# Optimization experiments

Measured on AMD Instinct MI355X. Metric: run time of the kernel, lower is better.

## Reference

```python
import jax, jax.numpy as jnp
import numpy as np

# Fixed hyperparameters from init_kwargs
KH, KW = 3, 3
GRID_SIZE = 5
SPLINE_ORDER = 3
GRID_RANGE = (-1.0, 1.0)


def _make_grid():
    # grid buffer: arange(-k, grid_size + k + 1) * h + grid_range[0], shape (G + 2k + 1,) = (12,)
    h = (GRID_RANGE[1] - GRID_RANGE[0]) / GRID_SIZE
    return (jnp.arange(-SPLINE_ORDER, GRID_SIZE + SPLINE_ORDER + 1, dtype=jnp.float32) * h
            + GRID_RANGE[0])


def _unfold(x):
    # torch.nn.Unfold with kernel (3,3), stride 1, pad 0, dilation 1.
    # Returns (N, C*KH*KW) with channel-major ordering (c, i, j), matching torch.
    B, C, H, W = x.shape
    Ho, Wo = H - KH + 1, W - KW + 1
    cols = [x[:, :, i:i + Ho, j:j + Wo] for i in range(KH) for j in range(KW)]
    p = jnp.stack(cols, axis=2)                    # (B, C, KH*KW, Ho, Wo)
    p = p.reshape(B, C * KH * KW, Ho * Wo)         # (B, in_features, L)
    p = p.transpose(0, 2, 1).reshape(-1, C * KH * KW)  # (B*L, in_features)
    return p, Ho, Wo


def _b_splines(x, grid):
    # x: (N, in_features); grid: (G + 2k + 1,) uniform, shared across features.
    # Returns (N, in_features, G + k) B-spline basis via Cox-de Boor recursion.
    x = x[..., None]  # (N, in, 1)
    bases = ((x >= grid[:-1]) & (x < grid[1:])).astype(x.dtype)  # (N, in, G+2k)
    for k in range(1, SPLINE_ORDER + 1):
        left = (x - grid[: -(k + 1)]) / (grid[k:-1] - grid[: -(k + 1)])
        right = (grid[k + 1:] - x) / (grid[k + 1:] - grid[1:-k])
        bases = left * bases[..., :-1] + right * bases[..., 1:]
    return bases  # (N, in, G + k)


def setup_inputs() -> dict:
    key = jax.random.key(0)
    k1, k2, k3, k4 = jax.random.split(key, 4)
    in_features = 32 * KH * KW  # 288
    out_features = 64
    n_coef = GRID_SIZE + SPLINE_ORDER  # 8
    x = jax.random.normal(k1, (16, 32, 64, 64), dtype=jnp.float32)
    base_weight = jax.random.normal(k2, (out_features, in_features), dtype=jnp.float32) * (1.0 / np.sqrt(in_features))
    spline_weight = jax.random.normal(k3, (out_features, in_features, n_coef), dtype=jnp.float32) * 0.1
    spline_scaler = jax.random.normal(k4, (out_features, in_features), dtype=jnp.float32) * (1.0 / np.sqrt(in_features))
    return {"x": x, "base_weight": base_weight, "spline_weight": spline_weight,
            "spline_scaler": spline_scaler}


def reference(x, base_weight, spline_weight, spline_scaler):
    B = x.shape[0]
    out_features = base_weight.shape[0]
    grid = _make_grid()

    patches, Ho, Wo = _unfold(x)                              # (N, in_features)
    N, in_features = patches.shape

    # KANLinear forward
    base_out = jnp.matmul(jax.nn.relu(patches), base_weight.T)  # (N, out)
    bases = _b_splines(patches, grid)                           # (N, in, G+k)
    scaled_w = spline_weight * spline_scaler[..., None]         # (out, in, G+k)
    spline_out = jnp.matmul(bases.reshape(N, -1), scaled_w.reshape(out_features, -1).T)
    out = base_out + spline_out                                 # (N, out)

    out = out.reshape(B, Ho, Wo, out_features).transpose(0, 3, 1, 2)  # (B, C_out, Ho, Wo)
    return out
```

## Files before the change

kernel.cpp:

```cpp
#include <hip/hip_runtime.h>
#include <stdint.h>

typedef _Float16 half8  __attribute__((ext_vector_type(8)));
typedef float    f32x4  __attribute__((ext_vector_type(4)));
typedef float    f32x16 __attribute__((ext_vector_type(16)));
typedef uint32_t u32x4  __attribute__((ext_vector_type(4)));

#define FIN  288
#define NOUT 64
#define LPB  3844
#define NBF  20736
#define NBAS (16*64*16*64*2)
#define NXR  (16*64*2*64*2)
#define PADS 16

#define SCL  200
#define LDSL (31*SCL + 2*64 + 64 + 8)


__device__ inline half8 bspline8(float xv) {
  float u = fmaf(xv, 2.5f, 5.5f);
  float fi = floorf(u);
  int i = (int)fi;
  float t = u - fi, s = 1.0f - t;
  float t2 = t * t, t3 = t2 * t;
  float s2 = s * s, s3 = s2 * s;
  float w3 = t3 * 0.16666667f;
  float w0 = s3 * 0.16666667f;
  float w1 = fmaf(0.5f, t3, -t2) + 0.66666667f;
  float w2 = fmaf(0.5f, s3, -s2) + 0.66666667f;
  uint32_t u01 = __builtin_bit_cast(uint32_t, __builtin_amdgcn_cvt_pkrtz(w0, w1));
  uint32_t u23 = __builtin_bit_cast(uint32_t, __builtin_amdgcn_cvt_pkrtz(w2, w3));
  uint64_t V = (uint64_t)u01 | ((uint64_t)u23 << 32);
  uint32_t vl = (uint32_t)(V << 16);
  u32x4 fr;
#pragma unroll
  for (int q = 0; q < 4; ++q) {
    int d = i - 2 * q;
    uint32_t rr = (uint32_t)(V >> ((48 - 16 * d) & 63));
    fr[q] = ((uint32_t)d <= 3u) ? rr : ((d == 4) ? vl : 0u);
  }
  return __builtin_bit_cast(half8, fr);
}

__global__ __launch_bounds__(256) void prep_all(const float* __restrict__ x,
                                                const float* __restrict__ bw,
                                                const float* __restrict__ sw,
                                                const float* __restrict__ sc,
                                                half8* __restrict__ ws) {
  int bid = blockIdx.x;
  if (bid < 8192) {
    int t = bid * 256 + threadIdx.x;
    int half = t & 1;
    int w    = (t >> 1) & 63;
    int u    = (t >> 7) & 15;
    int bh   = t >> 11;
    float xv = x[(size_t)(bh >> 6) * 131072 + (u * 2 + half) * 4096 +
                 (bh & 63) * 64 + w];
    ws[NBF + t] = bspline8(xv);
  } else if (bid < 9216) {
    int t = (bid - 8192) * 256 + threadIdx.x;
    int half = t & 1;
    int w    = (t >> 1) & 63;
    int u    = (t >> 7) & 1;
    int bh   = t >> 8;
    const float* xp = x + (size_t)(bh >> 6) * 131072 + (u * 16 + half * 8) * 4096 +
                      (bh & 63) * 64 + w;
    half8 v;
#pragma unroll
    for (int j = 0; j < 8; ++j) v[j] = (_Float16)fmaxf(xp[j * 4096], 0.0f);
    ws[NBF + NBAS + t] = v;
  } else {
    int t = (bid - 9216) * 256 + threadIdx.x;
    half8 v;
    int dst;
    if (t < NOUT * FIN) {
      int o = t / FIN;
      int f = t - o * FIN;
      float scale = sc[t];
      const float* p = sw + t * 8;
#pragma unroll
      for (int j = 0; j < 8; ++j) v[j] = (_Float16)(p[j] * scale);
      int c  = f / 9;
      int r  = f - c * 9;
      int ii = r / 3;
      int jj = r - ii * 3;
      int pp = ii * 3 + jj;
      int u  = c >> 1, half = c & 1;
      int nf = o >> 5, col = o & 31;
      dst = pp * 2048 + u * 128 + nf * 64 + half * 32 + col;
    } else {
      int t2 = t - NOUT * FIN;
      int lane = t2 & 63;
      int nf   = (t2 >> 6) & 1;
      int u    = (t2 >> 7) & 1;
      int pos  = t2 >> 8;
      int half = lane >> 5, col = lane & 31;
      int o = nf * 32 + col;
#pragma unroll
      for (int j = 0; j < 8; ++j)
        v[j] = (_Float16)bw[o * FIN + 9 * (u * 16 + half * 8 + j) + pos];
      dst = NOUT * FIN + t2;
    }
    ws[dst] = v;
  }
}

#define MFMA32(A, B, C) __builtin_amdgcn_mfma_f32_32x32x16_f16((A), (B), (C), 0, 0, 0)

#define LOAD_AF(PP, AF)                                                     \
  {                                                                         \
    const half8* pAf_ = bbS + ((PP) / 3) * 2048 + ((PP) % 3) * 2;           \
    _Pragma("unroll")                                                       \
    for (int uu = 0; uu < 8; ++uu) {                                        \
      AF[uu * 2]     = pAf_[(ulo + uu) * 128];                              \
      AF[uu * 2 + 1] = pAf_[(ulo + uu) * 128 + 64];                         \
    }                                                                       \
  }

#define PAIR(PP, AFC, AFN)                                                  \
  {                                                                         \
    half8 stg[4];                                                           \
    if ((PP) < 8) {                                                         \
      const half8* src_ = bfrag + ((PP) + 1) * 2048;                        \
      _Pragma("unroll")                                                     \
      for (int i = 0; i < 4; ++i) stg[i] = src_[i * 512 + tid];             \
      LOAD_AF((PP) + 1, AFN)                                                \
    }                                                                       \
    _Pragma("unroll")                                                       \
    for (int uu = 0; uu < 8; ++uu) {                                        \
      int u_ = ulo + uu;                                                    \
      _Pragma("unroll")                                                     \
      for (int nf = 0; nf < 2; ++nf) {                                      \
        half8 bf_ = bcur[u_ * 128 + nf * 64 + lane];                        \
        acc[0][nf] = MFMA32(AFC[uu * 2], bf_, acc[0][nf]);                  \
        acc[1][nf] = MFMA32(AFC[uu * 2 + 1], bf_, acc[1][nf]);              \
      }                                                                     \
    }                                                                       \
    if ((PP) < 8) {                                                         \
      _Pragma("unroll")                                                     \
      for (int i = 0; i < 4; ++i) balt[i * 512 + tid] = stg[i];             \
    }                                                                       \
    __syncthreads();                                                        \
    { half8* t_ = bcur; bcur = balt; balt = t_; }                           \
  }

#define BASE_LOAD(POS, A0, A1, B0, B1)                                      \
  {                                                                         \
    constexpr int i2_ = (POS) / 3, j2_ = (POS) - 3 * ((POS) / 3);           \
    const half8* pAf_ = xr + (size_t)((b * 64 + hoc + i2_) * 2 + g2) * 128 + \
                        j2_ * 2 + laneoff;                                  \
    A0 = pAf_[0];                                                           \
    A1 = pAf_[64];                                                          \
    const half8* bfp_ = bfrag + NOUT * FIN + ((POS) * 2 + g2) * 128 + lane; \
    B0 = bfp_[0];                                                           \
    B1 = bfp_[64];                                                          \
  }

#define BASE_MMA(A0, A1, B0, B1)                                            \
  {                                                                         \
    acc[0][0] = MFMA32(A0, B0, acc[0][0]);                                  \
    acc[1][0] = MFMA32(A1, B0, acc[1][0]);                                  \
    acc[0][1] = MFMA32(A0, B1, acc[0][1]);                                  \
    acc[1][1] = MFMA32(A1, B1, acc[1][1]);                                  \
  }

__global__ __launch_bounds__(512, 2) void kan_main(
    const half8* __restrict__ ws,
    float* __restrict__ out) {
  __shared__ __align__(16) unsigned char ldsraw[65536];
  half8* lbf0 = (half8*)ldsraw;
  half8* lbf1 = (half8*)(ldsraw + 32768);
  float* red  = (float*)ldsraw;

  const half8* __restrict__ bfrag = ws;
  const half8* __restrict__ bas   = ws + NBF;
  const half8* __restrict__ xr    = ws + NBF + NBAS;

  const int tid = threadIdx.x;
  int bid0 = blockIdx.x;
  int bid = (bid0 & 7) * 32 + (bid0 >> 3);
  const int b  = bid >> 4;
  const int hg = bid & 15;

  const int lane = tid & 63;
  const int wv   = tid >> 6;
  const int g2   = wv >> 2;
  const int rw   = wv & 3;
  const int l31  = lane & 31;
  const int lhi  = lane >> 5;
  const int laneoff = l31 * 2 + lhi;
  const int ho   = hg * 4 + rw;
  const int hoc  = ho < 61 ? ho : 61;
  const int ulo  = g2 * 8;

  f32x16 acc[2][2];
#pragma unroll
  for (int mt = 0; mt < 2; ++mt)
#pragma unroll
    for (int nf = 0; nf < 2; ++nf)
#pragma unroll
      for (int e = 0; e < 16; ++e) acc[mt][nf][e] = 0.f;

  const half8* bbS = bas + (size_t)(b * 64 + hoc) * 2048 + laneoff;

  half8 afA[16], afB[16];

#pragma unroll
  for (int i = 0; i < 4; ++i) {
    int idx = i * 512 + tid;
    lbf0[idx] = bfrag[idx];
  }
  LOAD_AF(0, afA)
  __syncthreads();
  half8* bcur = lbf0;
  half8* balt = lbf1;

  half8 bx0, bx1, bxb0, bxb1;
  half8 by0, by1, byb0, byb1;

  PAIR(0, afA, afB)
  PAIR(1, afB, afA)
  PAIR(2, afA, afB)
  PAIR(3, afB, afA)
  PAIR(4, afA, afB)
  PAIR(5, afB, afA)
  PAIR(6, afA, afB)
  PAIR(7, afB, afA)
  BASE_LOAD(0, bx0, bx1, bxb0, bxb1)
  PAIR(8, afA, afB)

  BASE_LOAD(1, by0, by1, byb0, byb1)
  BASE_MMA(bx0, bx1, bxb0, bxb1)
  BASE_LOAD(2, bx0, bx1, bxb0, bxb1)
  BASE_MMA(by0, by1, byb0, byb1)
  BASE_LOAD(3, by0, by1, byb0, byb1)
  BASE_MMA(bx0, bx1, bxb0, bxb1)
  BASE_LOAD(4, bx0, bx1, bxb0, bxb1)
  BASE_MMA(by0, by1, byb0, byb1)
  BASE_LOAD(5, by0, by1, byb0, byb1)
  BASE_MMA(bx0, bx1, bxb0, bxb1)
  BASE_LOAD(6, bx0, bx1, bxb0, bxb1)
  BASE_MMA(by0, by1, byb0, byb1)
  BASE_LOAD(7, by0, by1, byb0, byb1)
  BASE_MMA(bx0, bx1, bxb0, bxb1)
  BASE_LOAD(8, bx0, bx1, bxb0, bxb1)
  BASE_MMA(by0, by1, byb0, byb1)
  BASE_MMA(bx0, bx1, bxb0, bxb1)

  if (g2) {
    int base = (rw * 64 + lane) * 64;
#pragma unroll
    for (int mt = 0; mt < 2; ++mt)
#pragma unroll
      for (int nf = 0; nf < 2; ++nf)
#pragma unroll
        for (int q4 = 0; q4 < 4; ++q4) {
          int pos = ((mt * 8 + nf * 4 + q4) + lane) & 15;
          f32x4 ch = {acc[mt][nf][q4 * 4], acc[mt][nf][q4 * 4 + 1],
                      acc[mt][nf][q4 * 4 + 2], acc[mt][nf][q4 * 4 + 3]};
          *(f32x4*)&red[base + pos * 4] = ch;
        }
  }
  __syncthreads();

  if (!g2) {
    int base = (rw * 64 + lane) * 64;
#pragma unroll
    for (int mt = 0; mt < 2; ++mt)
#pragma unroll
      for (int nf = 0; nf < 2; ++nf)
#pragma unroll
        for (int q4 = 0; q4 < 4; ++q4) {
          int pos = ((mt * 8 + nf * 4 + q4) + lane) & 15;
          f32x4 ch = *(const f32x4*)&red[base + pos * 4];
          acc[mt][nf][q4 * 4]     += ch[0];
          acc[mt][nf][q4 * 4 + 1] += ch[1];
          acc[mt][nf][q4 * 4 + 2] += ch[2];
          acc[mt][nf][q4 * 4 + 3] += ch[3];
        }

    if (ho < 62) {
      float* ob = out + b * (NOUT * LPB) + ho * 62;
#pragma unroll
      for (int mt = 0; mt < 2; ++mt) {
#pragma unroll
        for (int reg = 0; reg < 16; ++reg) {
          int wo2 = mt * 32 + (reg & 3) + 8 * (reg >> 2) + 4 * lhi;
          if (wo2 < 62) {
#pragma unroll
            for (int nf = 0; nf < 2; ++nf) {
              int o = nf * 32 + l31;
              ob[o * LPB + wo2] = acc[mt][nf][reg];
            }
          }
        }
      }
    }
  }
}

#define KSPL 72
__global__ void prep_bfrag_legacy(const float* __restrict__ bw,
                                  const float* __restrict__ sw,
                                  const float* __restrict__ sc,
                                  half8* __restrict__ bfrag) {
  int t = blockIdx.x * 256 + threadIdx.x;
  half8 v;
  int dst;
  if (t < NOUT * FIN) {
    int o = t / FIN;
    int f = t - o * FIN;
    float scale = sc[t];
    const float* p = sw + t * 8;
#pragma unroll
    for (int c = 0; c < 8; ++c) v[c] = (_Float16)(p[c] * scale);
    int ch = f / 9;
    int r  = f - ch * 9;
    int ii = r / 3;
    int jj = r - ii * 3;
    int g  = ch >> 2, q = ch & 3;
    int kt = ii * 24 + jj * 8 + g;
    dst = (kt * 4 + (o >> 4)) * 64 + q * 16 + (o & 15);
  } else {
    int t2 = t - NOUT * FIN;
    int lane = t2 & 63;
    int nf = (t2 >> 6) & 3;
    int ktb = t2 >> 8;
    int o = nf * 16 + (lane & 15);
    int f0 = ktb * 32 + (lane >> 4) * 8;
    const float* p = bw + o * FIN + f0;
#pragma unroll
    for (int c = 0; c < 8; ++c) v[c] = (_Float16)p[c];
    dst = ((KSPL + ktb) * 4 + nf) * 64 + lane;
  }
  bfrag[dst] = v;
}

__global__ __launch_bounds__(256, 4) void kan_main_legacy(
    const float* __restrict__ x,
    const half8* __restrict__ bfrag,
    float* __restrict__ out) {
  __shared__ float lx[LDSL];
  const int tid = threadIdx.x;
  const int bid = blockIdx.x;
  const int b  = bid / 62;
  const int ho = bid - b * 62;
  const float* xb = x + b * 131072 + ho * 64;
#pragma unroll
  for (int r = 0; r < 6; ++r) {
    int gid = r * 256 + tid;
    int row = gid >> 4;
    int c   = (row * 683) >> 11;
    int ii  = row - c * 3;
    int colv = (gid & 15) * 4;
    const float4 v = *(const float4*)(xb + c * 4096 + ii * 64 + colv);
    *(float4*)(&lx[c * SCL + ii * 64 + colv]) = v;
  }
  __syncthreads();
  const int lane = tid & 63;
  const int wv   = tid >> 6;
  const int quad = lane >> 4;
  const int m16  = lane & 15;
  const int wo   = wv * 16 + m16;
  f32x4 acc[4];
#pragma unroll
  for (int nf = 0; nf < 4; ++nf) acc[nf] = (f32x4){0.f, 0.f, 0.f, 0.f};
  int kt = 0;
#pragma unroll
  for (int ii = 0; ii < 3; ++ii) {
#pragma unroll
    for (int jj = 0; jj < 3; ++jj) {
      const float* lbase = lx + quad * SCL + ii * 64 + wo + jj;
#pragma unroll
      for (int g = 0; g < 8; ++g) {
        float xv = lbase[g * (4 * SCL)];
        half8 af = bspline8(xv);
#pragma unroll
        for (int nf = 0; nf < 4; ++nf) {
          half8 bf = bfrag[(kt * 4 + nf) * 64 + lane];
          acc[nf] = __builtin_amdgcn_mfma_f32_16x16x32_f16(af, bf, acc[nf], 0, 0, 0);
        }
        ++kt;
      }
    }
  }
#pragma unroll
  for (int kb = 0; kb < 9; ++kb) {
    int f0 = kb * 32 + quad * 8;
    half8 a;
#pragma unroll
    for (int j = 0; j < 8; ++j) {
      int f = f0 + j;
      int c = (f * 57) >> 9;
      int r = f - c * 9;
      int i2 = (r * 11) >> 5;
      int j2 = r - i2 * 3;
      a[j] = (_Float16)fmaxf(lx[c * SCL + i2 * 64 + wo + j2], 0.0f);
    }
#pragma unroll
    for (int nf = 0; nf < 4; ++nf) {
      half8 bf = bfrag[((KSPL + kb) * 4 + nf) * 64 + lane];
      acc[nf] = __builtin_amdgcn_mfma_f32_16x16x32_f16(a, bf, acc[nf], 0, 0, 0);
    }
  }
  float* ob = out + b * (NOUT * LPB) + ho * 62;
#pragma unroll
  for (int rg = 0; rg < 4; ++rg) {
    int wo2 = wv * 16 + quad * 4 + rg;
    if (wo2 < 62) {
#pragma unroll
      for (int nf = 0; nf < 4; ++nf) {
        int o = nf * 16 + m16;
        ob[o * LPB + wo2] = acc[nf][rg];
      }
    }
  }
}

extern "C" void kernel_launch(void* const* d_in, const int* in_sizes, int n_in,
                              void* d_out, int out_size, void* d_ws, size_t ws_size,
                              hipStream_t stream) {
  const float* x  = (const float*)d_in[0];
  const float* bw = (const float*)d_in[1];
  const float* sw = (const float*)d_in[2];
  const float* sc = (const float*)d_in[3];
  float* out = (float*)d_out;
  half8* ws = (half8*)d_ws;

  const size_t need = (size_t)(NBF + NBAS + NXR + PADS) * sizeof(half8);
  if (ws_size >= need) {
    prep_all<<<9297, 256, 0, stream>>>(x, bw, sw, sc, ws);
    kan_main<<<256, 512, 0, stream>>>(ws, out);
  } else {
    prep_bfrag_legacy<<<81, 256, 0, stream>>>(bw, sw, sc, ws);
    kan_main_legacy<<<16 * 62, 256, 0, stream>>>(x, ws, out);
  }
}
```

Before: 117.5 us.

## Split output channels across waves and double block count in kan_main

Each wave now computes half of the 64 output channels (nh selects 32), and each block covers 2 output rows instead of 4. The grid doubles to 512 blocks and launch bounds rise to 4 blocks per CU, with accumulators halved to cut register pressure. The aim is more parallelism and occupancy across the 256 CUs. In exchange, each wave still loads the full A fragments, so A-fragment global traffic per output doubles. LDS use of 64KB per block may also cap how many blocks actually co-reside.

```diff
diff --git a/kernel.cpp b/kernel.cpp
--- a/kernel.cpp
+++ b/kernel.cpp
@@ -130,12 +130,9 @@
     _Pragma("unroll")                                                       \
     for (int uu = 0; uu < 8; ++uu) {                                        \
       int u_ = ulo + uu;                                                    \
-      _Pragma("unroll")                                                     \
-      for (int nf = 0; nf < 2; ++nf) {                                      \
-        half8 bf_ = bcur[u_ * 128 + nf * 64 + lane];                        \
-        acc[0][nf] = MFMA32(AFC[uu * 2], bf_, acc[0][nf]);                  \
-        acc[1][nf] = MFMA32(AFC[uu * 2 + 1], bf_, acc[1][nf]);              \
-      }                                                                     \
+      half8 bf_ = bcur[u_ * 128 + nhoff + lane];                            \
+      acc[0] = MFMA32(AFC[uu * 2], bf_, acc[0]);                            \
+      acc[1] = MFMA32(AFC[uu * 2 + 1], bf_, acc[1]);                        \
     }                                                                       \
     if ((PP) < 8) {                                                         \
       _Pragma("unroll")                                                     \
@@ -145,27 +142,23 @@
     { half8* t_ = bcur; bcur = balt; balt = t_; }                           \
   }
 
-#define BASE_LOAD(POS, A0, A1, B0, B1)                                      \
+#define BASE_LOAD(POS, A0, A1, B0)                                          \
   {                                                                         \
     constexpr int i2_ = (POS) / 3, j2_ = (POS) - 3 * ((POS) / 3);           \
     const half8* pAf_ = xr + (size_t)((b * 64 + hoc + i2_) * 2 + g2) * 128 + \
                         j2_ * 2 + laneoff;                                  \
     A0 = pAf_[0];                                                           \
     A1 = pAf_[64];                                                          \
-    const half8* bfp_ = bfrag + NOUT * FIN + ((POS) * 2 + g2) * 128 + lane; \
-    B0 = bfp_[0];                                                           \
-    B1 = bfp_[64];                                                          \
-  }
-
-#define BASE_MMA(A0, A1, B0, B1)                                            \
+    B0 = bfrag[NOUT * FIN + ((POS) * 2 + g2) * 128 + nhoff + lane];         \
+  }
+
+#define BASE_MMA(A0, A1, B0)                                                \
   {                                                                         \
-    acc[0][0] = MFMA32(A0, B0, acc[0][0]);                                  \
-    acc[1][0] = MFMA32(A1, B0, acc[1][0]);                                  \
-    acc[0][1] = MFMA32(A0, B1, acc[0][1]);                                  \
-    acc[1][1] = MFMA32(A1, B1, acc[1][1]);                                  \
-  }
-
-__global__ __launch_bounds__(512, 2) void kan_main(
+    acc[0] = MFMA32(A0, B0, acc[0]);                                        \
+    acc[1] = MFMA32(A1, B0, acc[1]);                                        \
+  }
+
+__global__ __launch_bounds__(512, 4) void kan_main(
     const half8* __restrict__ ws,
     float* __restrict__ out) {
   __shared__ __align__(16) unsigned char ldsraw[65536];
@@ -179,28 +172,28 @@
 
   const int tid = threadIdx.x;
   int bid0 = blockIdx.x;
-  int bid = (bid0 & 7) * 32 + (bid0 >> 3);
-  const int b  = bid >> 4;
-  const int hg = bid & 15;
+  int bid = (bid0 & 7) * 64 + (bid0 >> 3);
+  const int b  = bid >> 5;
+  const int hp = bid & 31;
 
   const int lane = tid & 63;
   const int wv   = tid >> 6;
-  const int g2   = wv >> 2;
-  const int rw   = wv & 3;
+  const int nh   = wv & 1;
+  const int g2   = (wv >> 1) & 1;
+  const int rw   = wv >> 2;
   const int l31  = lane & 31;
   const int lhi  = lane >> 5;
   const int laneoff = l31 * 2 + lhi;
-  const int ho   = hg * 4 + rw;
+  const int nhoff = nh * 64;
+  const int ho   = hp * 2 + rw;
   const int hoc  = ho < 61 ? ho : 61;
   const int ulo  = g2 * 8;
 
-  f32x16 acc[2][2];
+  f32x16 acc[2];
 #pragma unroll
   for (int mt = 0; mt < 2; ++mt)
 #pragma unroll
-    for (int nf = 0; nf < 2; ++nf)
-#pragma unroll
-      for (int e = 0; e < 16; ++e) acc[mt][nf][e] = 0.f;
+    for (int e = 0; e < 16; ++e) acc[mt][e] = 0.f;
 
   const half8* bbS = bas + (size_t)(b * 64 + hoc) * 2048 + laneoff;
 
@@ -216,8 +209,8 @@
   half8* bcur = lbf0;
   half8* balt = lbf1;
 
-  half8 bx0, bx1, bxb0, bxb1;
-  half8 by0, by1, byb0, byb1;
+  half8 bx0, bx1, bxb;
+  half8 by0, by1, byb;
 
   PAIR(0, afA, afB)
   PAIR(1, afB, afA)
@@ -227,72 +220,65 @@
   PAIR(5, afB, afA)
   PAIR(6, afA, afB)
   PAIR(7, afB, afA)
-  BASE_LOAD(0, bx0, bx1, bxb0, bxb1)
+  BASE_LOAD(0, bx0, bx1, bxb)
   PAIR(8, afA, afB)
 
-  BASE_LOAD(1, by0, by1, byb0, byb1)
-  BASE_MMA(bx0, bx1, bxb0, bxb1)
-  BASE_LOAD(2, bx0, bx1, bxb0, bxb1)
-  BASE_MMA(by0, by1, byb0, byb1)
-  BASE_LOAD(3, by0, by1, byb0, byb1)
-  BASE_MMA(bx0, bx1, bxb0, bxb1)
-  BASE_LOAD(4, bx0, bx1, bxb0, bxb1)
-  BASE_MMA(by0, by1, byb0, byb1)
-  BASE_LOAD(5, by0, by1, byb0, byb1)
-  BASE_MMA(bx0, bx1, bxb0, bxb1)
-  BASE_LOAD(6, bx0, bx1, bxb0, bxb1)
-  BASE_MMA(by0, by1, byb0, byb1)
-  BASE_LOAD(7, by0, by1, byb0, byb1)
-  BASE_MMA(bx0, bx1, bxb0, bxb1)
-  BASE_LOAD(8, bx0, bx1, bxb0, bxb1)
-  BASE_MMA(by0, by1, byb0, byb1)
-  BASE_MMA(bx0, bx1, bxb0, bxb1)
+  BASE_LOAD(1, by0, by1, byb)
+  BASE_MMA(bx0, bx1, bxb)
+  BASE_LOAD(2, bx0, bx1, bxb)
+  BASE_MMA(by0, by1, byb)
+  BASE_LOAD(3, by0, by1, byb)
+  BASE_MMA(bx0, bx1, bxb)
+  BASE_LOAD(4, bx0, bx1, bxb)
+  BASE_MMA(by0, by1, byb)
+  BASE_LOAD(5, by0, by1, byb)
+  BASE_MMA(bx0, bx1, bxb)
+  BASE_LOAD(6, bx0, bx1, bxb)
+  BASE_MMA(by0, by1, byb)
+  BASE_LOAD(7, by0, by1, byb)
+  BASE_MMA(bx0, bx1, bxb)
+  BASE_LOAD(8, bx0, bx1, bxb)
+  BASE_MMA(by0, by1, byb)
+  BASE_MMA(bx0, bx1, bxb)
 
   if (g2) {
-    int base = (rw * 64 + lane) * 64;
+    int base = ((rw * 2 + nh) * 64 + lane) * 64;
 #pragma unroll
     for (int mt = 0; mt < 2; ++mt)
 #pragma unroll
-      for (int nf = 0; nf < 2; ++nf)
-#pragma unroll
-        for (int q4 = 0; q4 < 4; ++q4) {
-          int pos = ((mt * 8 + nf * 4 + q4) + lane) & 15;
-          f32x4 ch = {acc[mt][nf][q4 * 4], acc[mt][nf][q4 * 4 + 1],
-                      acc[mt][nf][q4 * 4 + 2], acc[mt][nf][q4 * 4 + 3]};
-          *(f32x4*)&red[base + pos * 4] = ch;
-        }
+      for (int q4 = 0; q4 < 4; ++q4) {
+        int pos = ((mt * 4 + q4) + lane) & 15;
+        f32x4 ch = {acc[mt][q4 * 4], acc[mt][q4 * 4 + 1],
+                    acc[mt][q4 * 4 + 2], acc[mt][q4 * 4 + 3]};
+        *(f32x4*)&red[base + pos * 4] = ch;
+      }
   }
   __syncthreads();
 
   if (!g2) {
-    int base = (rw * 64 + lane) * 64;
+    int base = ((rw * 2 + nh) * 64 + lane) * 64;
 #pragma unroll
     for (int mt = 0; mt < 2; ++mt)
 #pragma unroll
-      for (int nf = 0; nf < 2; ++nf)
-#pragma unroll
-        for (int q4 = 0; q4 < 4; ++q4) {
-          int pos = ((mt * 8 + nf * 4 + q4) + lane) & 15;
-          f32x4 ch = *(const f32x4*)&red[base + pos * 4];
-          acc[mt][nf][q4 * 4]     += ch[0];
-          acc[mt][nf][q4 * 4 + 1] += ch[1];
-          acc[mt][nf][q4 * 4 + 2] += ch[2];
-          acc[mt][nf][q4 * 4 + 3] += ch[3];
-        }
+      for (int q4 = 0; q4 < 4; ++q4) {
+        int pos = ((mt * 4 + q4) + lane) & 15;
+        f32x4 ch = *(const f32x4*)&red[base + pos * 4];
+        acc[mt][q4 * 4]     += ch[0];
+        acc[mt][q4 * 4 + 1] += ch[1];
+        acc[mt][q4 * 4 + 2] += ch[2];
+        acc[mt][q4 * 4 + 3] += ch[3];
+      }
 
     if (ho < 62) {
       float* ob = out + b * (NOUT * LPB) + ho * 62;
+      const int o = nh * 32 + l31;
 #pragma unroll
       for (int mt = 0; mt < 2; ++mt) {
 #pragma unroll
         for (int reg = 0; reg < 16; ++reg) {
           int wo2 = mt * 32 + (reg & 3) + 8 * (reg >> 2) + 4 * lhi;
           if (wo2 < 62) {
-#pragma unroll
-            for (int nf = 0; nf < 2; ++nf) {
-              int o = nf * 32 + l31;
-              ob[o * LPB + wo2] = acc[mt][nf][reg];
-            }
+            ob[o * LPB + wo2] = acc[mt][reg];
           }
         }
       }
@@ -431,7 +417,7 @@
   const size_t need = (size_t)(NBF + NBAS + NXR + PADS) * sizeof(half8);
   if (ws_size >= need) {
     prep_all<<<9297, 256, 0, stream>>>(x, bw, sw, sc, ws);
-    kan_main<<<256, 512, 0, stream>>>(ws, out);
+    kan_main<<<512, 512, 0, stream>>>(ws, out);
   } else {
     prep_bfrag_legacy<<<81, 256, 0, stream>>>(bw, sw, sc, ws);
     kan_main_legacy<<<16 * 62, 256, 0, stream>>>(x, ws, out);
```

Measured after the change: 133.2 us. 13.3% more time.
